# Optimization experiments

Hardware: AMD Instinct MI355X
Metric: run time of the kernel (lower is better)

The kernel has to match this reference:

```python
import jax, jax.numpy as jnp
import numpy as np

B, T, F, U, H = 256, 512, 128, 256, 64


def setup_inputs() -> dict:
    key = jax.random.key(0)
    k0, k1, k2, k3, k4 = jax.random.split(key, 5)
    x = jax.random.normal(k0, (B, T, F), dtype=jnp.float32)
    # Keras RandomUniform default range (-0.05, 0.05) for LSTM kernel/bias
    kernel = jax.random.uniform(k1, (F, 4 * U), minval=-0.05, maxval=0.05, dtype=jnp.float32)
    rec_kernel = jax.random.uniform(k2, (U, 4 * U), minval=-0.05, maxval=0.05, dtype=jnp.float32)
    bias = jax.random.uniform(k3, (4 * U,), minval=-0.05, maxval=0.05, dtype=jnp.float32)
    # Dense head: glorot-ish scale for the big [T*U, H] weight
    w_out = jax.random.normal(k4, (T * U, H), dtype=jnp.float32) * (1.0 / np.sqrt(T * U))
    b_out = jnp.zeros((H,), dtype=jnp.float32)
    return {"x": x, "kernel": kernel, "rec_kernel": rec_kernel, "bias": bias,
            "w_out": w_out, "b_out": b_out}


def _lstm_swish(x, kernel, rec_kernel, bias):
    """Keras LSTM with activation=swish, recurrent_activation=sigmoid.
    Gate order along last axis: i, f, c(g), o. Returns full hidden sequence [B,T,U]."""
    b, t, _ = x.shape
    u = rec_kernel.shape[0]
    # Precompute input projections for all timesteps: [B,T,4U]
    xz = jnp.einsum('btf,fg->btg', x, kernel) + bias

    def step(carry, xz_t):
        h, c = carry
        z = xz_t + h @ rec_kernel  # [B,4U]
        zi, zf, zg, zo = jnp.split(z, 4, axis=-1)
        i = jax.nn.sigmoid(zi)
        f = jax.nn.sigmoid(zf)
        g = jax.nn.swish(zg)
        o = jax.nn.sigmoid(zo)
        c_new = f * c + i * g
        h_new = o * jax.nn.swish(c_new)
        return (h_new, c_new), h_new

    h0 = jnp.zeros((b, u), dtype=x.dtype)
    c0 = jnp.zeros((b, u), dtype=x.dtype)
    (_, _), hs = jax.lax.scan(step, (h0, c0), jnp.swapaxes(xz, 0, 1))  # hs: [T,B,U]
    return jnp.swapaxes(hs, 0, 1)  # [B,T,U]


def reference(x, kernel, rec_kernel, bias, w_out, b_out):
    seq = _lstm_swish(x, kernel, rec_kernel, bias)        # [B,T,U]
    flat = seq.reshape(seq.shape[0], -1)                   # [B,T*U]
    return flat @ w_out + b_out                            # [B,horizon]
```

## Files before the change

kernel.cpp:

```cpp
#include <hip/hip_runtime.h>
#include <stdint.h>

#define B_ 256
#define T_ 512
#define F_ 128
#define U_ 256
#define H_ 64
#define G4U (4 * U_)

typedef __attribute__((ext_vector_type(8))) short short8;
typedef __attribute__((ext_vector_type(4))) float f32x4;
typedef unsigned long long ull;

#define BARRIER_LDS() asm volatile("s_waitcnt lgkmcnt(0)\ns_barrier" ::: "memory")

__device__ __forceinline__ uint16_t f2bf(float f) {
  uint32_t u = __builtin_bit_cast(uint32_t, f);
  u += 0x7fffu + ((u >> 16) & 1u);
  return (uint16_t)(u >> 16);
}
__device__ __forceinline__ float sigm(float z) {
  return 1.0f / (1.0f + __expf(-z));
}
__device__ __forceinline__ ull ald(const ull* p) {
  return __hip_atomic_load(p, __ATOMIC_RELAXED, __HIP_MEMORY_SCOPE_AGENT);
}

__global__ __launch_bounds__(512, 2) void lstm_kernel(
    const float* __restrict__ x, const float* __restrict__ kern,
    const float* __restrict__ rker, const float* __restrict__ bias,
    uint16_t* __restrict__ seq, ull* __restrict__ hbuf)
{
  const int tid  = threadIdx.x;
  const int lane = tid & 63;
  const int wv   = tid >> 6;
  const int il   = lane & 15;
  const int rg   = lane >> 4;
  const int bg   = blockIdx.x & 15;
  const int m    = blockIdx.x >> 4;

  __shared__ __align__(16) uint16_t x_stage[4][64][8];
  __shared__ __align__(16) uint16_t h_stage[2][8][64][8];
  __shared__ __align__(16) uint16_t kern_lds[8192 * 8];

  short8 wf[4][8];
  float  bias_r[4];
  #pragma unroll
  for (int q = 0; q < 4; ++q) {
    const int gcol = q * U_ + m * 128 + wv * 16 + il;
    bias_r[q] = bias[gcol];
    #pragma unroll
    for (int kk = 0; kk < 8; ++kk) {
      const int ktg = ((kk & 4) ? (m ^ 1) : m) * 4 + (kk & 3);
      short8 v;
      #pragma unroll
      for (int j = 0; j < 8; ++j)
        v[j] = (short)f2bf(rker[(size_t)(ktg * 32 + rg * 8 + j) * G4U + gcol]);
      wf[q][kk] = v;
    }
  }

  for (int s = 0; s < 16; ++s) {
    const int slot = tid + s * 512;
    const int ln = slot & 63, kt = (slot >> 6) & 3, ct = slot >> 8;
    const int col = (ct >> 3) * U_ + m * 128 + (ct & 7) * 16 + (ln & 15);
    const int kb  = kt * 32 + (ln >> 4) * 8;
    short8 v;
    #pragma unroll
    for (int j = 0; j < 8; ++j)
      v[j] = (short)f2bf(kern[(size_t)(kb + j) * G4U + col]);
    *(short8*)&kern_lds[(size_t)slot * 8] = v;
  }

  const int xkt = tid >> 7;
  const int xln = (tid >> 1) & 63;
  const int xj0 = (tid & 1) * 4;
  const int xrow = xln & 15;
  const int xk0  = xkt * 32 + (xln >> 4) * 8 + xj0;

  const int Ua  = m * 128 + wv * 16 + il;
  const int kta = Ua >> 5, ga = ((Ua & 31) >> 3) * 16, posa = Ua & 7;

  ull* const pub_s  = hbuf + (size_t)(bg * 2 + m) * 2048;
  const ull* const pub_p  = hbuf + (size_t)(bg * 2 + (m ^ 1)) * 2048;

  float cst[4];
  #pragma unroll
  for (int j = 0; j < 4; ++j) cst[j] = 0.f;

  float xp[4];
  {
    const float* p = x + ((size_t)(bg * 16 + xrow) * T_ + 0) * F_ + xk0;
    #pragma unroll
    for (int j = 0; j < 4; ++j) xp[j] = p[j];
    uint16_t* d = (uint16_t*)x_stage + tid * 4;
    #pragma unroll
    for (int j = 0; j < 4; ++j) d[j] = f2bf(xp[j]);
  }
  __syncthreads();

  for (int t = 0; t < T_; ++t) {
    const ull* pp = pub_p + (size_t)((t - 1) & 1) * 1024 + tid * 2;
    ull pv0, pv1;
    if (t > 0) { pv0 = ald(pp); pv1 = ald(pp + 1); }
    __builtin_amdgcn_sched_barrier(0);
    {
      const int tn = (t + 1 < T_) ? t + 1 : t;
      const float* p = x + ((size_t)(bg * 16 + xrow) * T_ + tn) * F_ + xk0;
      #pragma unroll
      for (int j = 0; j < 4; ++j) xp[j] = p[j];
    }
    f32x4 acc[4];
    #pragma unroll
    for (int q = 0; q < 4; ++q)
      acc[q] = (f32x4){bias_r[q], bias_r[q], bias_r[q], bias_r[q]};
    #pragma unroll
    for (int kt = 0; kt < 4; ++kt) {
      short8 a = *(const short8*)&x_stage[kt][lane][0];
      #pragma unroll
      for (int q = 0; q < 4; ++q) {
        short8 b = *(const short8*)&kern_lds[(size_t)(((q * 8 + wv) * 4 + kt) * 64 + lane) * 8];
        acc[q] = __builtin_amdgcn_mfma_f32_16x16x32_bf16(a, b, acc[q], 0, 0, 0);
      }
    }
    if (t > 0) {
      const int p_ = (t - 1) & 1;
      #pragma unroll
      for (int kk = 0; kk < 4; ++kk) {
        short8 a = *(const short8*)&h_stage[p_][m * 4 + kk][lane][0];
        #pragma unroll
        for (int q = 0; q < 4; ++q)
          acc[q] = __builtin_amdgcn_mfma_f32_16x16x32_bf16(a, wf[q][kk], acc[q], 0, 0, 0);
      }
      const uint32_t expt = (uint32_t)t;
      while (((uint32_t)(pv0 >> 32) != expt) | ((uint32_t)(pv1 >> 32) != expt)) {
        pv0 = ald(pp); pv1 = ald(pp + 1);
      }
      const int u_loc = tid >> 2;
      const int U  = (m ^ 1) * 128 + u_loc;
      const int kt = U >> 5, g = ((U & 31) >> 3) * 16, pos = U & 7;
      const int rb = (tid & 3) * 4;
      h_stage[p_][kt][g + rb + 0][pos] = (uint16_t)pv0;
      h_stage[p_][kt][g + rb + 1][pos] = (uint16_t)(pv0 >> 16);
      h_stage[p_][kt][g + rb + 2][pos] = (uint16_t)pv1;
      h_stage[p_][kt][g + rb + 3][pos] = (uint16_t)(pv1 >> 16);
    }
    BARRIER_LDS();
    if (t > 0) {
      const int p_ = (t - 1) & 1;
      #pragma unroll
      for (int kk = 0; kk < 4; ++kk) {
        short8 a = *(const short8*)&h_stage[p_][(m ^ 1) * 4 + kk][lane][0];
        #pragma unroll
        for (int q = 0; q < 4; ++q)
          acc[q] = __builtin_amdgcn_mfma_f32_16x16x32_bf16(a, wf[q][4 + kk], acc[q], 0, 0, 0);
      }
    }
    {
      uint16_t* d = (uint16_t*)x_stage + tid * 4;
      #pragma unroll
      for (int j = 0; j < 4; ++j) d[j] = f2bf(xp[j]);
    }
    {
      uint16_t b16[4];
      #pragma unroll
      for (int j = 0; j < 4; ++j) {
        const float zi = acc[0][j], zf = acc[1][j];
        const float zg = acc[2][j], zo = acc[3][j];
        const float ii = sigm(zi), ff = sigm(zf);
        const float gg = zg * sigm(zg), oo = sigm(zo);
        const float c  = ff * cst[j] + ii * gg;
        cst[j] = c;
        b16[j] = f2bf(oo * (c * sigm(c)));
      }
      const int s2 = t & 1;
      ull* pw = pub_s + (size_t)s2 * 1024 + (size_t)(wv * 16 + il) * 8 + rg * 2;
      const ull tg = (ull)(uint32_t)(t + 1) << 32;
      __hip_atomic_store(pw,     (ull)((uint32_t)b16[0] | ((uint32_t)b16[1] << 16)) | tg,
                         __ATOMIC_RELAXED, __HIP_MEMORY_SCOPE_AGENT);
      __hip_atomic_store(pw + 1, (ull)((uint32_t)b16[2] | ((uint32_t)b16[3] << 16)) | tg,
                         __ATOMIC_RELAXED, __HIP_MEMORY_SCOPE_AGENT);
      #pragma unroll
      for (int j = 0; j < 4; ++j) {
        h_stage[s2][kta][ga + rg * 4 + j][posa] = b16[j];
        seq[((size_t)(bg * 16 + rg * 4 + j) * T_ + t) * U_ + Ua] = b16[j];
      }
    }
    BARRIER_LDS();
  }
}

__global__ __launch_bounds__(256, 1) void head_kernel(
    const uint16_t* __restrict__ seq, const float* __restrict__ w_out,
    float* __restrict__ partials)
{
  const int g    = blockIdx.x;
  const int tid  = threadIdx.x;
  const int lane = tid & 63;
  const int wv   = tid >> 6;

  f32x4 acc[4][4];
  #pragma unroll
  for (int i = 0; i < 4; ++i)
    #pragma unroll
    for (int c = 0; c < 4; ++c) acc[i][c] = (f32x4){0.f, 0.f, 0.f, 0.f};

  for (int ks = 0; ks < 64; ++ks) {
    const int krow = g * 2048 + ks * 32 + (lane >> 4) * 8;
    short8 bf[4];
    #pragma unroll
    for (int c = 0; c < 4; ++c) {
      short8 v;
      #pragma unroll
      for (int j = 0; j < 8; ++j)
        v[j] = (short)f2bf(w_out[(size_t)(krow + j) * H_ + c * 16 + (lane & 15)]);
      bf[c] = v;
    }
    #pragma unroll
    for (int i = 0; i < 4; ++i) {
      const int b = (wv * 4 + i) * 16 + (lane & 15);
      short8 a = *(const short8*)(seq + (size_t)b * (T_ * U_) + krow);
      #pragma unroll
      for (int c = 0; c < 4; ++c)
        acc[i][c] = __builtin_amdgcn_mfma_f32_16x16x32_bf16(a, bf[c], acc[i][c], 0, 0, 0);
    }
  }
  #pragma unroll
  for (int i = 0; i < 4; ++i)
    #pragma unroll
    for (int c = 0; c < 4; ++c)
      #pragma unroll
      for (int r = 0; r < 4; ++r) {
        const int b = wv * 64 + i * 16 + (lane >> 4) * 4 + r;
        partials[((size_t)g * B_ + b) * H_ + c * 16 + (lane & 15)] = acc[i][c][r];
      }
}

__global__ void reduce_kernel(const float* __restrict__ partials,
                              const float* __restrict__ b_out,
                              float* __restrict__ out)
{
  const int i = blockIdx.x * 256 + threadIdx.x;
  float s = b_out[i & (H_ - 1)];
  #pragma unroll 8
  for (int g = 0; g < 64; ++g) s += partials[(size_t)g * (B_ * H_) + i];
  out[i] = s;
}

extern "C" void kernel_launch(void* const* d_in, const int* in_sizes, int n_in,
                              void* d_out, int out_size, void* d_ws, size_t ws_size,
                              hipStream_t stream) {
  (void)in_sizes; (void)n_in; (void)out_size; (void)ws_size;
  const float* x     = (const float*)d_in[0];
  const float* kern  = (const float*)d_in[1];
  const float* rker  = (const float*)d_in[2];
  const float* bias  = (const float*)d_in[3];
  const float* w_out = (const float*)d_in[4];
  const float* b_out = (const float*)d_in[5];
  float* out = (float*)d_out;

  char* ws = (char*)d_ws;
  const size_t seq_bytes  = (size_t)B_ * T_ * U_ * 2;
  const size_t hbuf_bytes = (size_t)32 * 2048 * 8;
  uint16_t* seq      = (uint16_t*)ws;
  ull*      hbuf     = (ull*)(ws + seq_bytes);
  float*    partials = (float*)(ws + seq_bytes + hbuf_bytes);

  hipMemsetAsync(hbuf, 0, hbuf_bytes, stream);

  lstm_kernel<<<32, 512, 0, stream>>>(x, kern, rker, bias, seq, hbuf);
  head_kernel<<<64, 256, 0, stream>>>(seq, w_out, partials);
  reduce_kernel<<<64, 256, 0, stream>>>(partials, b_out, out);
}
```

Measured before the change: 1.286 ms.

## Precompute input projections in a parallel kernel and interleave four batch chunks per LSTM block

Moves the x@kernel input projection out of the serial recurrence into a separate, widely parallel kernel that writes bf16 gate pre-activations to workspace. The recurrent kernel then runs on 8 blocks, each handling four 16-row batch chunks in turn, so one chunk's cross-block h exchange can overlap another chunk's MFMA work. Handshakes now use tagged 64-bit values with spin-wait. The gain depends on the overlap hiding exchange latency. The cost is an extra large workspace buffer written and then streamed back each step, plus far fewer CUs doing the serial recurrence. A fallback keeps the old path when the workspace is too small.

```diff
diff --git a/kernel.cpp b/kernel.cpp
--- a/kernel.cpp
+++ b/kernel.cpp
@@ -19,6 +19,9 @@
   u += 0x7fffu + ((u >> 16) & 1u);
   return (uint16_t)(u >> 16);
 }
+__device__ __forceinline__ float bf2f(uint32_t v) {
+  return __builtin_bit_cast(float, (v & 0xffffu) << 16);
+}
 __device__ __forceinline__ float sigm(float z) {
   return 1.0f / (1.0f + __expf(-z));
 }
@@ -26,7 +29,231 @@
   return __hip_atomic_load(p, __ATOMIC_RELAXED, __HIP_MEMORY_SCOPE_AGENT);
 }
 
-__global__ __launch_bounds__(512, 2) void lstm_kernel(
+__global__ __launch_bounds__(256, 1) void xz_pre_kernel(
+    const float* __restrict__ x, const float* __restrict__ kern,
+    const float* __restrict__ bias, uint16_t* __restrict__ xz)
+{
+  const int tid  = threadIdx.x;
+  const int lane = tid & 63;
+  const int q    = tid >> 6;
+  const int il   = lane & 15;
+  const int bgm  = blockIdx.x & 31;
+  const int tc   = blockIdx.x >> 5;
+  const int bg   = bgm >> 1, m = bgm & 1;
+
+  __shared__ __align__(16) uint16_t kern_lds[8192 * 8];
+  __shared__ __align__(16) uint16_t x_stage[2][4][64][8];
+
+  for (int s = 0; s < 32; ++s) {
+    const int slot = tid + s * 256;
+    const int ln = slot & 63, kt = (slot >> 6) & 3, ctq = slot >> 8;
+    const int col = (ctq >> 3) * U_ + m * 128 + (ctq & 7) * 16 + (ln & 15);
+    const int kb  = kt * 32 + (ln >> 4) * 8;
+    short8 v;
+    #pragma unroll
+    for (int j = 0; j < 8; ++j)
+      v[j] = (short)f2bf(kern[(size_t)(kb + j) * G4U + col]);
+    *(short8*)&kern_lds[(size_t)slot * 8] = v;
+  }
+  float bias_r[8];
+  #pragma unroll
+  for (int ct = 0; ct < 8; ++ct)
+    bias_r[ct] = bias[q * U_ + m * 128 + ct * 16 + il];
+
+  const int xrow = tid & 15, xfb = (tid >> 4) * 8;
+  const int xs_kt = xfb >> 5, xs_l = (((xfb & 31) >> 3) * 16) + xrow;
+
+  float xv[8];
+  {
+    const float* p = x + ((size_t)(bg * 16 + xrow) * T_ + tc * 64) * F_ + xfb;
+    #pragma unroll
+    for (int j = 0; j < 8; ++j) xv[j] = p[j];
+  }
+  __syncthreads();
+
+  for (int tt = 0; tt < 64; ++tt) {
+    const int t = tc * 64 + tt;
+    const int bb = tt & 1;
+    {
+      uint16_t* d = &x_stage[bb][xs_kt][xs_l][0];
+      #pragma unroll
+      for (int j = 0; j < 8; ++j) d[j] = f2bf(xv[j]);
+    }
+    BARRIER_LDS();
+    {
+      const int tn = (tt + 1 < 64) ? t + 1 : t;
+      const float* p = x + ((size_t)(bg * 16 + xrow) * T_ + tn) * F_ + xfb;
+      #pragma unroll
+      for (int j = 0; j < 8; ++j) xv[j] = p[j];
+    }
+    f32x4 acc[8];
+    #pragma unroll
+    for (int ct = 0; ct < 8; ++ct)
+      acc[ct] = (f32x4){bias_r[ct], bias_r[ct], bias_r[ct], bias_r[ct]};
+    #pragma unroll
+    for (int kt = 0; kt < 4; ++kt) {
+      short8 a = *(const short8*)&x_stage[bb][kt][lane][0];
+      #pragma unroll
+      for (int ct = 0; ct < 8; ++ct) {
+        short8 b = *(const short8*)&kern_lds[(size_t)(((q * 8 + ct) * 4 + kt) * 64 + lane) * 8];
+        acc[ct] = __builtin_amdgcn_mfma_f32_16x16x32_bf16(a, b, acc[ct], 0, 0, 0);
+      }
+    }
+    uint16_t* ob = xz + ((size_t)bgm * T_ + t) * 8192;
+    #pragma unroll
+    for (int ct = 0; ct < 8; ++ct) {
+      const uint32_t lo = (uint32_t)f2bf(acc[ct][0]) | ((uint32_t)f2bf(acc[ct][1]) << 16);
+      const uint32_t hi = (uint32_t)f2bf(acc[ct][2]) | ((uint32_t)f2bf(acc[ct][3]) << 16);
+      *(ull*)(ob + (size_t)((ct * 4 + q) * 64 + lane) * 4) = (ull)lo | ((ull)hi << 32);
+    }
+  }
+}
+
+__global__ __launch_bounds__(512, 2) void lstm4_kernel(
+    const float* __restrict__ rker, uint16_t* __restrict__ seq,
+    ull* __restrict__ hbuf, const uint16_t* __restrict__ xz)
+{
+  const int tid  = threadIdx.x;
+  const int lane = tid & 63;
+  const int wv   = tid >> 6;
+  const int il   = lane & 15;
+  const int rg   = lane >> 4;
+  const int pair = blockIdx.x & 3;
+  const int m    = blockIdx.x >> 2;
+
+  __shared__ __align__(16) uint16_t h_stage[4][2][8][64][8];
+
+  short8 wf[4][8];
+  #pragma unroll
+  for (int q = 0; q < 4; ++q) {
+    const int gcol = q * U_ + m * 128 + wv * 16 + il;
+    #pragma unroll
+    for (int kk = 0; kk < 8; ++kk) {
+      const int ktg = ((kk & 4) ? (m ^ 1) : m) * 4 + (kk & 3);
+      short8 v;
+      #pragma unroll
+      for (int j = 0; j < 8; ++j)
+        v[j] = (short)f2bf(rker[(size_t)(ktg * 32 + rg * 8 + j) * G4U + gcol]);
+      wf[q][kk] = v;
+    }
+  }
+
+  const int u_loc = wv * 16 + il;
+  const int Ua = m * 128 + u_loc;
+  const int kta = Ua >> 5, ga = ((Ua & 31) >> 3) * 16, posa = Ua & 7;
+  const int up_u = tid >> 2;
+  const int Up = (m ^ 1) * 128 + up_u;
+  const int up_kt = Up >> 5, up_g = ((Up & 31) >> 3) * 16, up_pos = Up & 7;
+  const int up_rb = (tid & 3) * 4;
+
+  ull* const pub0 = hbuf + (size_t)pair * 8192 + (size_t)m * 2048;
+  const ull* const peer0 = hbuf + (size_t)pair * 8192 + (size_t)(m ^ 1) * 2048;
+
+  const uint16_t* const xzbase = xz + (size_t)(pair * 8 + m) * ((size_t)T_ * 8192);
+  const size_t xzthr = (size_t)(wv * 4) * 256 + (size_t)lane * 4;
+
+  float cst[4][4];
+  #pragma unroll
+  for (int c = 0; c < 4; ++c)
+    #pragma unroll
+    for (int j = 0; j < 4; ++j) cst[c][j] = 0.f;
+
+  ull xzp[2][4];
+  #pragma unroll
+  for (int q = 0; q < 4; ++q) {
+    xzp[0][q] = *(const ull*)(xzbase + (size_t)0 * 8388608 + xzthr + q * 256);
+    xzp[1][q] = *(const ull*)(xzbase + (size_t)1 * 8388608 + xzthr + q * 256);
+  }
+
+  for (int t = 0; t < T_; ++t) {
+    const int p_ = (t - 1) & 1;
+    const uint32_t expt = (uint32_t)t;
+    const ull* pl0 = peer0 + (size_t)p_ * 1024 + tid * 2;
+    ull pvv[4][2];
+    if (t > 0) {
+      #pragma unroll
+      for (int c = 0; c < 4; ++c) {
+        pvv[c][0] = ald(pl0 + (size_t)c * 4096);
+        pvv[c][1] = ald(pl0 + (size_t)c * 4096 + 1);
+      }
+    }
+    #pragma unroll
+    for (int c = 0; c < 4; ++c) {
+      f32x4 acc[4];
+      #pragma unroll
+      for (int q = 0; q < 4; ++q) {
+        const uint32_t w0 = (uint32_t)xzp[c & 1][q];
+        const uint32_t w1 = (uint32_t)(xzp[c & 1][q] >> 32);
+        acc[q][0] = bf2f(w0); acc[q][1] = bf2f(w0 >> 16);
+        acc[q][2] = bf2f(w1); acc[q][3] = bf2f(w1 >> 16);
+      }
+      {
+        const int cn = (c + 2) & 3;
+        const int tn = (c < 2) ? t : ((t + 1 < T_) ? t + 1 : t);
+        const uint16_t* pb = xzbase + (size_t)cn * 8388608 + (size_t)tn * 8192 + xzthr;
+        #pragma unroll
+        for (int q = 0; q < 4; ++q)
+          xzp[c & 1][q] = *(const ull*)(pb + q * 256);
+      }
+      if (t > 0) {
+        #pragma unroll
+        for (int kk = 0; kk < 4; ++kk) {
+          short8 a = *(const short8*)&h_stage[c][p_][m * 4 + kk][lane][0];
+          #pragma unroll
+          for (int q = 0; q < 4; ++q)
+            acc[q] = __builtin_amdgcn_mfma_f32_16x16x32_bf16(a, wf[q][kk], acc[q], 0, 0, 0);
+        }
+        const ull* pp = pl0 + (size_t)c * 4096;
+        while (((uint32_t)(pvv[c][0] >> 32) != expt) | ((uint32_t)(pvv[c][1] >> 32) != expt)) {
+          pvv[c][0] = ald(pp); pvv[c][1] = ald(pp + 1);
+        }
+        const uint32_t d0 = (uint32_t)pvv[c][0], d1 = (uint32_t)pvv[c][1];
+        h_stage[c][p_][up_kt][up_g + up_rb + 0][up_pos] = (uint16_t)d0;
+        h_stage[c][p_][up_kt][up_g + up_rb + 1][up_pos] = (uint16_t)(d0 >> 16);
+        h_stage[c][p_][up_kt][up_g + up_rb + 2][up_pos] = (uint16_t)d1;
+        h_stage[c][p_][up_kt][up_g + up_rb + 3][up_pos] = (uint16_t)(d1 >> 16);
+      }
+      BARRIER_LDS();
+      if (t > 0) {
+        #pragma unroll
+        for (int kk = 0; kk < 4; ++kk) {
+          short8 a = *(const short8*)&h_stage[c][p_][(m ^ 1) * 4 + kk][lane][0];
+          #pragma unroll
+          for (int q = 0; q < 4; ++q)
+            acc[q] = __builtin_amdgcn_mfma_f32_16x16x32_bf16(a, wf[q][4 + kk], acc[q], 0, 0, 0);
+        }
+      }
+      uint16_t b16[4];
+      #pragma unroll
+      for (int j = 0; j < 4; ++j) {
+        const float zi = acc[0][j], zf = acc[1][j];
+        const float zg = acc[2][j], zo = acc[3][j];
+        const float ii = sigm(zi), ff = sigm(zf);
+        const float gg = zg * sigm(zg), oo = sigm(zo);
+        const float cc = ff * cst[c][j] + ii * gg;
+        cst[c][j] = cc;
+        b16[j] = f2bf(oo * (cc * sigm(cc)));
+      }
+      {
+        const int s2 = t & 1;
+        ull* pw = pub0 + (size_t)c * 4096 + (size_t)s2 * 1024
+                       + (size_t)u_loc * 8 + rg * 2;
+        const ull tg = (ull)(uint32_t)(t + 1) << 32;
+        __hip_atomic_store(pw,     (ull)((uint32_t)b16[0] | ((uint32_t)b16[1] << 16)) | tg,
+                           __ATOMIC_RELAXED, __HIP_MEMORY_SCOPE_AGENT);
+        __hip_atomic_store(pw + 1, (ull)((uint32_t)b16[2] | ((uint32_t)b16[3] << 16)) | tg,
+                           __ATOMIC_RELAXED, __HIP_MEMORY_SCOPE_AGENT);
+        #pragma unroll
+        for (int j = 0; j < 4; ++j) {
+          h_stage[c][s2][kta][ga + rg * 4 + j][posa] = b16[j];
+          seq[((size_t)((pair * 4 + c) * 16 + rg * 4 + j) * T_ + t) * U_ + Ua] = b16[j];
+        }
+      }
+    }
+  }
+}
+
+__global__ __launch_bounds__(512, 2) void lstm_fallback(
     const float* __restrict__ x, const float* __restrict__ kern,
     const float* __restrict__ rker, const float* __restrict__ bias,
     uint16_t* __restrict__ seq, ull* __restrict__ hbuf)
@@ -59,7 +286,6 @@
       wf[q][kk] = v;
     }
   }
-
   for (int s = 0; s < 16; ++s) {
     const int slot = tid + s * 512;
     const int ln = slot & 63, kt = (slot >> 6) & 3, ct = slot >> 8;
@@ -71,23 +297,18 @@
       v[j] = (short)f2bf(kern[(size_t)(kb + j) * G4U + col]);
     *(short8*)&kern_lds[(size_t)slot * 8] = v;
   }
-
   const int xkt = tid >> 7;
   const int xln = (tid >> 1) & 63;
   const int xj0 = (tid & 1) * 4;
   const int xrow = xln & 15;
   const int xk0  = xkt * 32 + (xln >> 4) * 8 + xj0;
-
   const int Ua  = m * 128 + wv * 16 + il;
   const int kta = Ua >> 5, ga = ((Ua & 31) >> 3) * 16, posa = Ua & 7;
-
-  ull* const pub_s  = hbuf + (size_t)(bg * 2 + m) * 2048;
-  const ull* const pub_p  = hbuf + (size_t)(bg * 2 + (m ^ 1)) * 2048;
-
+  ull* const pub_s = hbuf + (size_t)(bg * 2 + m) * 2048;
+  const ull* const pub_p = hbuf + (size_t)(bg * 2 + (m ^ 1)) * 2048;
   float cst[4];
   #pragma unroll
   for (int j = 0; j < 4; ++j) cst[j] = 0.f;
-
   float xp[4];
   {
     const float* p = x + ((size_t)(bg * 16 + xrow) * T_ + 0) * F_ + xk0;
@@ -98,12 +319,13 @@
     for (int j = 0; j < 4; ++j) d[j] = f2bf(xp[j]);
   }
   __syncthreads();
-
   for (int t = 0; t < T_; ++t) {
     const ull* pp = pub_p + (size_t)((t - 1) & 1) * 1024 + tid * 2;
-    ull pv0, pv1;
-    if (t > 0) { pv0 = ald(pp); pv1 = ald(pp + 1); }
-    __builtin_amdgcn_sched_barrier(0);
+    ull pv0 = 0, pv1 = 0;
+    if (t > 0) {
+      pv0 = ald(pp); pv1 = ald(pp + 1);
+      __builtin_amdgcn_sched_barrier(0);
+    }
     {
       const int tn = (t + 1 < T_) ? t + 1 : t;
       const float* p = x + ((size_t)(bg * 16 + xrow) * T_ + tn) * F_ + xk0;
@@ -250,7 +472,7 @@
 extern "C" void kernel_launch(void* const* d_in, const int* in_sizes, int n_in,
                               void* d_out, int out_size, void* d_ws, size_t ws_size,
                               hipStream_t stream) {
-  (void)in_sizes; (void)n_in; (void)out_size; (void)ws_size;
+  (void)in_sizes; (void)n_in; (void)out_size;
   const float* x     = (const float*)d_in[0];
   const float* kern  = (const float*)d_in[1];
   const float* rker  = (const float*)d_in[2];
@@ -262,13 +484,22 @@
   char* ws = (char*)d_ws;
   const size_t seq_bytes  = (size_t)B_ * T_ * U_ * 2;
   const size_t hbuf_bytes = (size_t)32 * 2048 * 8;
+  const size_t part_bytes = (size_t)64 * B_ * H_ * 4;
+  const size_t xz_bytes   = (size_t)32 * T_ * 8192 * 2;
   uint16_t* seq      = (uint16_t*)ws;
   ull*      hbuf     = (ull*)(ws + seq_bytes);
   float*    partials = (float*)(ws + seq_bytes + hbuf_bytes);
+  uint16_t* xzbuf    = (uint16_t*)(ws + seq_bytes + hbuf_bytes + part_bytes);
+  const size_t need  = seq_bytes + hbuf_bytes + part_bytes + xz_bytes;
 
   hipMemsetAsync(hbuf, 0, hbuf_bytes, stream);
 
-  lstm_kernel<<<32, 512, 0, stream>>>(x, kern, rker, bias, seq, hbuf);
+  if (ws_size >= need) {
+    xz_pre_kernel<<<256, 256, 0, stream>>>(x, kern, bias, xzbuf);
+    lstm4_kernel<<<8, 512, 0, stream>>>(rker, seq, hbuf, xzbuf);
+  } else {
+    lstm_fallback<<<32, 512, 0, stream>>>(x, kern, rker, bias, seq, hbuf);
+  }
   head_kernel<<<64, 256, 0, stream>>>(seq, w_out, partials);
   reduce_kernel<<<64, 256, 0, stream>>>(partials, b_out, out);
 }
```

New measurement: 1.292 ms. About the same (+0.4%).
